# Optimization experiments

Measured on AMD Instinct MI355X. Metric: run time of the kernel, lower is better.

Reference implementation:

```python
import jax, jax.numpy as jnp
import numpy as np

EMBED = 2048
N_HEAD = 32
N_KV = 8
HEAD_DIM = 64
GROUP = N_HEAD // N_KV


def _rope_tables(seq_len, head_dim):
    inv_freq = 1.0 / (10000.0 ** (jnp.arange(0, head_dim, 2, dtype=jnp.float32) / head_dim))
    ang = jnp.arange(seq_len, dtype=jnp.float32)[:, None] * inv_freq[None, :]  # [S, D/2]
    ang = jnp.concatenate([ang, ang], axis=-1)  # [S, D]
    return jnp.cos(ang), jnp.sin(ang)


def apply_rope(x, cos, sin, offset=0):
    # x: [B, H, S, D]
    S, D = x.shape[2], x.shape[3]
    x1, x2 = x[..., : D // 2], x[..., D // 2 :]
    c = cos[offset : offset + S][None, None]
    s = sin[offset : offset + S][None, None]
    rotated = jnp.concatenate([-x2, x1], axis=-1)
    return (x * c + rotated * s).astype(x.dtype)


def setup_inputs() -> dict:
    key = jax.random.key(0)
    kx, kq, kk, kv, ko = jax.random.split(key, 5)
    B, S = 2, 2048
    x = jax.random.normal(kx, (B, S, EMBED), dtype=jnp.float32)
    mask = jnp.triu(jnp.ones((S, S), dtype=bool), k=1)  # causal: True = masked
    cos, sin = _rope_tables(S, HEAD_DIM)
    std = 0.02
    Wq = jax.random.normal(kq, (EMBED, EMBED), dtype=jnp.float32) * std
    Wk = jax.random.normal(kk, (EMBED, N_KV * HEAD_DIM), dtype=jnp.float32) * std
    Wv = jax.random.normal(kv, (EMBED, N_KV * HEAD_DIM), dtype=jnp.float32) * std
    Wo = jax.random.normal(ko, (EMBED, EMBED), dtype=jnp.float32) * std
    return {"x": x, "mask": mask, "cos": cos, "sin": sin,
            "Wq": Wq, "Wk": Wk, "Wv": Wv, "Wo": Wo}


def reference(x, mask, cos, sin, Wq, Wk, Wv, Wo):
    B, S, E = x.shape
    # projections (no bias)
    q = (x @ Wq).reshape(B, S, N_HEAD, HEAD_DIM).transpose(0, 2, 1, 3)  # [B,H,S,D]
    k = (x @ Wk).reshape(B, S, N_KV, HEAD_DIM).transpose(0, 2, 1, 3)    # [B,G,S,D]
    v = (x @ Wv).reshape(B, S, N_KV, HEAD_DIM).transpose(0, 2, 1, 3)    # [B,G,S,D]
    q = apply_rope(q, cos, sin, offset=0)
    k = apply_rope(k, cos, sin, offset=0)
    next_k, next_v = k, v  # kv cache to return
    # GQA: head h uses kv group h // GROUP; avoid repeat_interleave via reshape
    qg = q.reshape(B, N_KV, GROUP, S, HEAD_DIM)
    scores = jnp.einsum('bgjsd,bgtd->bgjst', qg, k) / np.float32(np.sqrt(HEAD_DIM))
    scores = jnp.where(mask[None, None, None], -jnp.inf, scores)
    attn = jax.nn.softmax(scores, axis=-1)
    out = jnp.einsum('bgjst,bgtd->bgjsd', attn, v)          # [B,G,group,S,D]
    out = out.reshape(B, N_HEAD, S, HEAD_DIM).transpose(0, 2, 1, 3).reshape(B, S, E)
    return out @ Wo, next_k, next_v
```

## Files before the change

### kernel.cpp

```cpp
#include <hip/hip_runtime.h>
#include <hip/hip_bf16.h>
#include <math.h>

#define NH 32
#define NKV 8
#define HD 64
#define B_ 2
#define S_ 2048
#define E_ 2048
#define M_ 4096

typedef unsigned short ushort_t;
typedef __attribute__((ext_vector_type(8))) short short8;
typedef __attribute__((ext_vector_type(4))) short short4v;
typedef __attribute__((ext_vector_type(4))) float floatx4;

__device__ inline unsigned short f2bf(float f) {
  unsigned int u = __float_as_uint(f);
  return (unsigned short)((u + 0x7FFFu + ((u >> 16) & 1u)) >> 16);
}

__device__ inline float fexp2(float x) {
  float r;
  asm("v_exp_f32 %0, %1" : "=v"(r) : "v"(x));
  return r;
}

__device__ inline void ld_lds16(const void* g, void* l) {
  __builtin_amdgcn_global_load_lds((__attribute__((address_space(1))) void*)g,
                                   (__attribute__((address_space(3))) void*)l, 16, 0, 0);
}

__device__ inline void transp32(const float* __restrict__ in, ushort_t* __restrict__ out,
                                int R, int C, int bx, int by, int tid, float (*tile)[33]) {
  int c0 = bx * 32, r0 = by * 32;
  int x = tid & 31, y0 = tid >> 5;
  for (int i = 0; i < 4; i++) {
    int r = y0 + i * 8;
    tile[r][x] = in[(size_t)(r0 + r) * C + c0 + x];
  }
  __syncthreads();
  for (int i = 0; i < 4; i++) {
    int r = y0 + i * 8;
    out[(size_t)(c0 + r) * R + r0 + x] = f2bf(tile[x][r]);
  }
}

__global__ __launch_bounds__(256) void prep(const float* __restrict__ x,
                                            ushort_t* __restrict__ xb,
                                            const float* __restrict__ Wq,
                                            const float* __restrict__ Wk,
                                            const float* __restrict__ Wv,
                                            ushort_t* __restrict__ WT) {
  __shared__ float tile[32][33];
  int bid = blockIdx.x, tid = threadIdx.x;
  if (bid < 4096) {
    size_t i = ((size_t)bid * 256 + tid) * 8;
    float4 a = *(const float4*)(x + i);
    float4 b = *(const float4*)(x + i + 4);
    short8 o;
    o[0] = (short)f2bf(a.x); o[1] = (short)f2bf(a.y);
    o[2] = (short)f2bf(a.z); o[3] = (short)f2bf(a.w);
    o[4] = (short)f2bf(b.x); o[5] = (short)f2bf(b.y);
    o[6] = (short)f2bf(b.z); o[7] = (short)f2bf(b.w);
    *(short8*)(xb + i) = o;
    return;
  }
  bid -= 4096;
  if (bid < 4096) { transp32(Wq, WT, 2048, 2048, bid & 63, bid >> 6, tid, tile); return; }
  bid -= 4096;
  if (bid < 1024) { transp32(Wk, WT + 2048 * 2048, 2048, 512, bid & 15, bid >> 4, tid, tile); return; }
  bid -= 1024;
  transp32(Wv, WT + 2560 * 2048, 2048, 512, bid & 15, bid >> 4, tid, tile);
}

__global__ __launch_bounds__(512) void gemm_qkv(const ushort_t* __restrict__ xb,
                                                const ushort_t* __restrict__ WT,
                                                ushort_t* __restrict__ qbf,
                                                float* __restrict__ outk,
                                                ushort_t* __restrict__ kbf,
                                                float* __restrict__ outv,
                                                ushort_t* __restrict__ vt,
                                                const float* __restrict__ cosP,
                                                const float* __restrict__ sinP) {
  __shared__ __align__(16) ushort_t L8[2][2][2][128][64];
  char* Lb = (char*)L8;
  int bid = blockIdx.x;
  int xcd = bid & 7, ii = bid >> 3;
  int mg = xcd >> 1, ng = xcd & 1;
  int m0 = (mg * 4 + ii / 6) * 256;
  int n0 = (ng * 6 + ii % 6) * 256;
  int tid = threadIdx.x;
  int w8 = tid >> 6, lane = tid & 63;
  int wrq = w8 >> 1, wcq = w8 & 1;
  int lr = lane & 15, quad = lane >> 4;
  int sx = lr & 7;
  int srow = w8 * 16 + (lane >> 3);
  int schunk = (lane & 7) ^ (lane >> 3);
  const char* abase = (const char*)(xb + (size_t)m0 * 2048);
  const char* bbase = (const char*)(WT + (size_t)n0 * 2048);
  floatx4 acc[4][2][4] = {};

#define STG(T, U)                                                                        \
  do {                                                                                   \
    const int mat_ = (U)&1, half_ = (U) >> 1;                                            \
    const char* sp = (mat_ ? bbase : abase) + (size_t)(half_ * 128 + srow) * 4096 +      \
                     (size_t)(T)*128 + schunk * 16;                                      \
    char* dp = Lb + (((T)&1) * 65536) + mat_ * 32768 + half_ * 16384 + w8 * 2048;        \
    ld_lds16(sp, dp);                                                                    \
    ld_lds16(sp + (size_t)8 * 4096, dp + 1024);                                          \
  } while (0)

#define PH(T, P, MH_, NH_, WAITS, DOSTAGE)                                               \
  do {                                                                                   \
    asm volatile(WAITS ::: "memory");                                                    \
    const char* Ab_ = Lb + (((T)&1) * 65536) + (MH_)*16384;                              \
    const char* Bb_ = Lb + (((T)&1) * 65536) + 32768 + (NH_)*16384;                      \
    short8 af_[2][2], bf_[4][2];                                                         \
    _Pragma("unroll") for (int i = 0; i < 2; i++) {                                      \
      size_t rb = (size_t)(wrq * 32 + i * 16 + lr) * 128;                                \
      _Pragma("unroll") for (int ks = 0; ks < 2; ks++)                                   \
          af_[i][ks] = *(const short8*)(Ab_ + rb + (((ks * 4 + quad) ^ sx) << 4));       \
    }                                                                                    \
    _Pragma("unroll") for (int j = 0; j < 4; j++) {                                      \
      size_t rb = (size_t)(wcq * 64 + j * 16 + lr) * 128;                                \
      _Pragma("unroll") for (int ks = 0; ks < 2; ks++)                                   \
          bf_[j][ks] = *(const short8*)(Bb_ + rb + (((ks * 4 + quad) ^ sx) << 4));       \
    }                                                                                    \
    if (DOSTAGE) STG((T) + 1, P);                                                        \
    __builtin_amdgcn_s_setprio(1);                                                       \
    _Pragma("unroll") for (int i = 0; i < 2; i++) _Pragma("unroll") for (int j = 0;      \
                                                                         j < 4; j++) {  \
      acc[P][i][j] =                                                                     \
          __builtin_amdgcn_mfma_f32_16x16x32_bf16(af_[i][0], bf_[j][0], acc[P][i][j],    \
                                                  0, 0, 0);                              \
      acc[P][i][j] =                                                                     \
          __builtin_amdgcn_mfma_f32_16x16x32_bf16(af_[i][1], bf_[j][1], acc[P][i][j],    \
                                                  0, 0, 0);                              \
    }                                                                                    \
    __builtin_amdgcn_s_setprio(0);                                                       \
  } while (0)

  STG(0, 0); STG(0, 1); STG(0, 2); STG(0, 3);

  for (int kt = 0; kt < 31; kt++) {
    PH(kt, 0, 0, 0, "s_waitcnt vmcnt(4)\n\ts_barrier", 1);
    PH(kt, 1, 1, 0, "s_waitcnt vmcnt(4)\n\ts_barrier", 1);
    PH(kt, 2, 1, 1, "s_waitcnt vmcnt(4)\n\ts_barrier", 1);
    PH(kt, 3, 0, 1, "s_barrier", 1);
  }
  PH(31, 0, 0, 0, "s_waitcnt vmcnt(4)\n\ts_barrier", 0);
  PH(31, 1, 1, 0, "s_waitcnt vmcnt(2)\n\ts_barrier", 0);
  PH(31, 2, 1, 1, "s_waitcnt vmcnt(0)\n\ts_barrier", 0);
  PH(31, 3, 0, 1, "s_barrier", 0);
#undef STG
#undef PH

  const int MHs[4] = {0, 1, 1, 0}, NHs[4] = {0, 0, 1, 1};
  if (n0 < 2048) {
    const float QS = 0.125f * 1.4426950408889634f;
#pragma unroll
    for (int p = 0; p < 4; p++)
#pragma unroll
      for (int i = 0; i < 2; i++)
#pragma unroll
        for (int j = 0; j < 2; j++) {
          int d = j * 16 + lr;
#pragma unroll
          for (int r = 0; r < 4; r++) {
            int row = m0 + MHs[p] * 128 + wrq * 32 + i * 16 + quad * 4 + r;
            int s = row & (S_ - 1);
            float c = cosP[s * 64 + d], sn = sinP[s * 64 + d];
            float x1 = acc[p][i][j][r], x2 = acc[p][i][j + 2][r];
            size_t oo = (size_t)row * 2048 + n0 + NHs[p] * 128 + wcq * 64 + d;
            qbf[oo] = f2bf((x1 * c - x2 * sn) * QS);
            qbf[oo + 32] = f2bf((x2 * c + x1 * sn) * QS);
          }
        }
  } else if (n0 < 2560) {
#pragma unroll
    for (int p = 0; p < 4; p++) {
      int h = ((n0 - 2048) >> 6) + NHs[p] * 2 + wcq;
#pragma unroll
      for (int i = 0; i < 2; i++)
#pragma unroll
        for (int j = 0; j < 2; j++) {
          int d = j * 16 + lr;
#pragma unroll
          for (int r = 0; r < 4; r++) {
            int row = m0 + MHs[p] * 128 + wrq * 32 + i * 16 + quad * 4 + r;
            int s = row & (S_ - 1), b = row >> 11;
            float c = cosP[s * 64 + d], sn = sinP[s * 64 + d];
            float x1 = acc[p][i][j][r], x2 = acc[p][i][j + 2][r];
            float y1 = x1 * c - x2 * sn, y2 = x2 * c + x1 * sn;
            size_t rowb = ((size_t)(b * NKV + h) * S_ + s) * 64;
            int xr = (s & 7) << 3;
            outk[rowb + d] = y1; outk[rowb + d + 32] = y2;
            kbf[rowb + (d ^ xr)] = f2bf(y1);
            kbf[rowb + ((d + 32) ^ xr)] = f2bf(y2);
          }
        }
    }
  } else {
#pragma unroll
    for (int p = 0; p < 4; p++) {
      int h = ((n0 - 2560) >> 6) + NHs[p] * 2 + wcq;
#pragma unroll
      for (int i = 0; i < 2; i++)
#pragma unroll
        for (int j = 0; j < 4; j++) {
          int d = j * 16 + lr;
          int row0 = m0 + MHs[p] * 128 + wrq * 32 + i * 16 + quad * 4;
          int s0 = row0 & (S_ - 1), b = row0 >> 11;
#pragma unroll
          for (int r = 0; r < 4; r++)
            outv[((size_t)(b * NKV + h) * S_ + s0 + r) * 64 + d] = acc[p][i][j][r];
          int tt = s0 >> 6, s4 = s0 & 63;
          short4v u;
          u[0] = (short)f2bf(acc[p][i][j][0]); u[1] = (short)f2bf(acc[p][i][j][1]);
          u[2] = (short)f2bf(acc[p][i][j][2]); u[3] = (short)f2bf(acc[p][i][j][3]);
          *(short4v*)(vt + ((size_t)(b * NKV + h) * 32 + tt) * 4096 + d * 64 +
                      (s4 ^ ((d & 7) << 3))) = u;
        }
    }
  }
}

__device__ __forceinline__ void gemm128_core(const ushort_t* __restrict__ Ag,
                                             const ushort_t* __restrict__ Bg,
                                             floatx4 (&acc)[4][4]) {
  __shared__ __align__(16) ushort_t As[2][128][64];
  __shared__ __align__(16) ushort_t Bs[2][128][64];
  int tid = threadIdx.x;
  int w = tid >> 6, lane = tid & 63;
  int wm = (w >> 1) * 64, wn = (w & 1) * 64;
  int lr = lane & 15, quad = lane >> 4;
  int sx = lr & 7;
  char* Asb = (char*)As;
  char* Bsb = (char*)Bs;

  size_t so[4];
#pragma unroll
  for (int s = 0; s < 4; s++)
    so[s] = (size_t)(w * 32 + s * 8 + (lane >> 3)) * 4096 + (size_t)(((lane & 7) ^ (lane >> 3)) * 16);
  const char* abase = (const char*)Ag;
  const char* bbase = (const char*)Bg;

#define STAGE128(buf, kt)                                          \
  do {                                                             \
    size_t ko = (size_t)(kt) * 128;                                \
    char* Ad = Asb + (buf) * 16384 + w * 4096;                     \
    char* Bd = Bsb + (buf) * 16384 + w * 4096;                     \
    _Pragma("unroll") for (int s = 0; s < 4; s++) {                \
      ld_lds16(abase + so[s] + ko, Ad + s * 1024);                 \
      ld_lds16(bbase + so[s] + ko, Bd + s * 1024);                 \
    }                                                              \
  } while (0)

  STAGE128(0, 0);
  __syncthreads();

  int cur = 0;
  for (int kt = 0; kt < 32; kt++) {
    if (kt < 31) STAGE128(cur ^ 1, kt + 1);
    const char* Ab = Asb + cur * 16384;
    const char* Bb = Bsb + cur * 16384;
    short8 af[4][2], bfr[4][2];
#pragma unroll
    for (int i = 0; i < 4; i++) {
      size_t rb = (size_t)(wm + i * 16 + lr) * 128;
#pragma unroll
      for (int ks = 0; ks < 2; ks++)
        af[i][ks] = *(const short8*)(Ab + rb + (((ks * 4 + quad) ^ sx) << 4));
    }
#pragma unroll
    for (int j = 0; j < 4; j++) {
      size_t rb = (size_t)(wn + j * 16 + lr) * 128;
#pragma unroll
      for (int ks = 0; ks < 2; ks++)
        bfr[j][ks] = *(const short8*)(Bb + rb + (((ks * 4 + quad) ^ sx) << 4));
    }
#pragma unroll
    for (int i = 0; i < 4; i++)
#pragma unroll
      for (int j = 0; j < 4; j++) {
        acc[i][j] = __builtin_amdgcn_mfma_f32_16x16x32_bf16(af[i][0], bfr[j][0], acc[i][j], 0, 0, 0);
        acc[i][j] = __builtin_amdgcn_mfma_f32_16x16x32_bf16(af[i][1], bfr[j][1], acc[i][j], 0, 0, 0);
      }
    __syncthreads();
    cur ^= 1;
  }
#undef STAGE128
}

__global__ __launch_bounds__(256) void gemm_o(const ushort_t* __restrict__ ctx,
                                              const ushort_t* __restrict__ WoT,
                                              float* __restrict__ y) {
  int o = blockIdx.y * 16 + blockIdx.x;
  int xcd = o & 7, i = o >> 3;
  int mg = xcd >> 1, ng = xcd & 1;
  int m0 = (mg * 8 + (i >> 3)) * 128;
  int n0 = (ng * 8 + (i & 7)) * 128;
  int tid = threadIdx.x;
  int w = tid >> 6, lane = tid & 63;
  int wm = (w >> 1) * 64, wn = (w & 1) * 64;
  int lr = lane & 15, quad = lane >> 4;

  floatx4 acc[4][4] = {};
  gemm128_core(ctx + (size_t)m0 * 2048, WoT + (size_t)n0 * 2048, acc);

#pragma unroll
  for (int i2 = 0; i2 < 4; i2++)
#pragma unroll
    for (int j = 0; j < 4; j++) {
      int row = m0 + wm + i2 * 16 + quad * 4;
      int col = n0 + wn + j * 16 + lr;
#pragma unroll
      for (int r = 0; r < 4; r++)
        y[(size_t)(row + r) * 2048 + col] = acc[i2][j][r];
    }
}

__global__ __launch_bounds__(256, 3) void attn2(ushort_t* __restrict__ q,
                                                const ushort_t* __restrict__ k,
                                                const ushort_t* __restrict__ vt,
                                                const float* __restrict__ Wo,
                                                ushort_t* __restrict__ WoT) {
  __shared__ __align__(16) ushort_t KV[2][2][64][64];
  __shared__ __align__(16) ushort_t Ps[4][2][16][64];
  __shared__ float tile[32][33];
  int bid0 = blockIdx.x;
  int tid = threadIdx.x;
  if (bid0 >= 1024) {
    int bid2 = bid0 - 1024;
    transp32(Wo, WoT, 2048, 2048, bid2 & 63, bid2 >> 6, tid, tile);
    return;
  }
  int bh = bid0 & 63;
  int qi = 15 - (bid0 >> 6);
  int b = bh >> 5, h = bh & 31, g = h >> 2;
  int w = tid >> 6, lane = tid & 63;
  int lr = lane & 15, quad = lane >> 4;

  int qg0 = qi * 128 + w * 16 + lr;
  int qg1 = qg0 + 64;
  short8 a00, a01, a10, a11;
  {
    const ushort_t* qp0 = q + ((size_t)(b * S_ + qg0) * NH + h) * HD;
    const ushort_t* qp1 = q + ((size_t)(b * S_ + qg1) * NH + h) * HD;
    a00 = *(const short8*)(qp0 + quad * 8);
    a01 = *(const short8*)(qp0 + 32 + quad * 8);
    a10 = *(const short8*)(qp1 + quad * 8);
    a11 = *(const short8*)(qp1 + 32 + quad * 8);
  }
  floatx4 od0[4] = {}, od1[4] = {};
  float mi0 = -INFINITY, li0 = 0.f, mi1 = -INFINITY, li1 = 0.f;

  const char* ksrc = (const char*)(k + (size_t)(b * NKV + g) * S_ * HD) + w * 2048 + lane * 16;
  const char* vsrc = (const char*)(vt + (size_t)(b * NKV + g) * S_ * HD) + w * 2048 + lane * 16;
  char* dB = (char*)&KV[0][0][0][0] + w * 2048;

  int sw = (lr & 7) << 4;
  int ro0 = (quad * 16) ^ sw;
  int ro1 = (64 + quad * 16) ^ sw;
  char* Pw = (char*)&Ps[0][0][0][0] + w * 4096;

  ld_lds16(ksrc, dB);
  ld_lds16(ksrc + 1024, dB + 1024);
  ld_lds16(vsrc, dB + 8192);
  ld_lds16(vsrc + 1024, dB + 8192 + 1024);
  asm volatile("s_waitcnt vmcnt(0)" ::: "memory");
  __syncthreads();

  int T = 2 * qi + 2;
  int cur = 0;
  for (int t = 0; t < T; t++) {
    if (t + 1 < T) {
      const char* kn = ksrc + (size_t)(t + 1) * 8192;
      const char* vn = vsrc + (size_t)(t + 1) * 8192;
      char* d = dB + (cur ^ 1) * 16384;
      ld_lds16(kn, d); ld_lds16(kn + 1024, d + 1024);
      ld_lds16(vn, d + 8192); ld_lds16(vn + 1024, d + 8192 + 1024);
    }
    const char* Kb = (const char*)&KV[cur][0][0][0];
    const char* Vb = (const char*)&KV[cur][1][0][0];
    bool dq0 = (t == 2 * qi);
    bool skip0 = (t == 2 * qi + 1);
    if (!skip0) {
      floatx4 sc[4];
      __builtin_amdgcn_s_setprio(1);
#pragma unroll
      for (int kn = 0; kn < 4; kn++) {
        short8 k0 = *(const short8*)(Kb + (kn * 16 + lr) * 128 + ro0);
        short8 k1 = *(const short8*)(Kb + (kn * 16 + lr) * 128 + ro1);
        floatx4 c = {};
        c = __builtin_amdgcn_mfma_f32_16x16x32_bf16(k0, a00, c, 0, 0, 0);
        c = __builtin_amdgcn_mfma_f32_16x16x32_bf16(k1, a01, c, 0, 0, 0);
        sc[kn] = c;
      }
      __builtin_amdgcn_s_setprio(0);
      float pv[16];
#pragma unroll
      for (int kn = 0; kn < 4; kn++)
#pragma unroll
        for (int r = 0; r < 4; r++) pv[kn * 4 + r] = sc[kn][r];
      if (dq0) {
#pragma unroll
        for (int e = 0; e < 16; e++) {
          int kg = t * 64 + (e >> 2) * 16 + quad * 4 + (e & 3);
          if (kg > qg0) pv[e] = -INFINITY;
        }
      }
      float m01 = fmaxf(pv[0], pv[1]),  m23 = fmaxf(pv[2], pv[3]);
      float m45 = fmaxf(pv[4], pv[5]),  m67 = fmaxf(pv[6], pv[7]);
      float m89 = fmaxf(pv[8], pv[9]),  mab = fmaxf(pv[10], pv[11]);
      float mcd = fmaxf(pv[12], pv[13]), mef = fmaxf(pv[14], pv[15]);
      float mx = fmaxf(fmaxf(fmaxf(m01, m23), fmaxf(m45, m67)),
                       fmaxf(fmaxf(m89, mab), fmaxf(mcd, mef)));
      mx = fmaxf(mx, __shfl_xor(mx, 16));
      mx = fmaxf(mx, __shfl_xor(mx, 32));
      if (__any(mx > mi0 + 11.5f)) {
        float mn = fmaxf(mi0, mx);
        float al = fexp2(mi0 - mn);
        li0 *= al;
#pragma unroll
        for (int dn = 0; dn < 4; dn++) {
          od0[dn][0] *= al; od0[dn][1] *= al; od0[dn][2] *= al; od0[dn][3] *= al;
        }
        mi0 = mn;
      }
      float ps = 0.f;
#pragma unroll
      for (int e = 0; e < 16; e++) {
        pv[e] = fexp2(pv[e] - mi0);
        ps += pv[e];
      }
      ps += __shfl_xor(ps, 16);
      ps += __shfl_xor(ps, 32);
      li0 += ps;
#pragma unroll
      for (int kn = 0; kn < 4; kn++) {
        unsigned int u0, u1;
        asm("v_cvt_pk_bf16_f32 %0, %1, %2" : "=v"(u0) : "v"(pv[kn * 4 + 0]), "v"(pv[kn * 4 + 1]));
        asm("v_cvt_pk_bf16_f32 %0, %1, %2" : "=v"(u1) : "v"(pv[kn * 4 + 2]), "v"(pv[kn * 4 + 3]));
        uint2 uu; uu.x = u0; uu.y = u1;
        *(uint2*)(Pw + lr * 128 + ((kn * 32 + quad * 8) ^ sw)) = uu;
      }
    }
    {
      floatx4 sc[4];
      __builtin_amdgcn_s_setprio(1);
#pragma unroll
      for (int kn = 0; kn < 4; kn++) {
        short8 k0 = *(const short8*)(Kb + (kn * 16 + lr) * 128 + ro0);
        short8 k1 = *(const short8*)(Kb + (kn * 16 + lr) * 128 + ro1);
        floatx4 c = {};
        c = __builtin_amdgcn_mfma_f32_16x16x32_bf16(k0, a10, c, 0, 0, 0);
        c = __builtin_amdgcn_mfma_f32_16x16x32_bf16(k1, a11, c, 0, 0, 0);
        sc[kn] = c;
      }
      __builtin_amdgcn_s_setprio(0);
      float pv[16];
#pragma unroll
      for (int kn = 0; kn < 4; kn++)
#pragma unroll
        for (int r = 0; r < 4; r++) pv[kn * 4 + r] = sc[kn][r];
      if (skip0) {
#pragma unroll
        for (int e = 0; e < 16; e++) {
          int kg = t * 64 + (e >> 2) * 16 + quad * 4 + (e & 3);
          if (kg > qg1) pv[e] = -INFINITY;
        }
      }
      float m01 = fmaxf(pv[0], pv[1]),  m23 = fmaxf(pv[2], pv[3]);
      float m45 = fmaxf(pv[4], pv[5]),  m67 = fmaxf(pv[6], pv[7]);
      float m89 = fmaxf(pv[8], pv[9]),  mab = fmaxf(pv[10], pv[11]);
      float mcd = fmaxf(pv[12], pv[13]), mef = fmaxf(pv[14], pv[15]);
      float mx = fmaxf(fmaxf(fmaxf(m01, m23), fmaxf(m45, m67)),
                       fmaxf(fmaxf(m89, mab), fmaxf(mcd, mef)));
      mx = fmaxf(mx, __shfl_xor(mx, 16));
      mx = fmaxf(mx, __shfl_xor(mx, 32));
      if (__any(mx > mi1 + 11.5f)) {
        float mn = fmaxf(mi1, mx);
        float al = fexp2(mi1 - mn);
        li1 *= al;
#pragma unroll
        for (int dn = 0; dn < 4; dn++) {
          od1[dn][0] *= al; od1[dn][1] *= al; od1[dn][2] *= al; od1[dn][3] *= al;
        }
        mi1 = mn;
      }
      float ps = 0.f;
#pragma unroll
      for (int e = 0; e < 16; e++) {
        pv[e] = fexp2(pv[e] - mi1);
        ps += pv[e];
      }
      ps += __shfl_xor(ps, 16);
      ps += __shfl_xor(ps, 32);
      li1 += ps;
#pragma unroll
      for (int kn = 0; kn < 4; kn++) {
        unsigned int u0, u1;
        asm("v_cvt_pk_bf16_f32 %0, %1, %2" : "=v"(u0) : "v"(pv[kn * 4 + 0]), "v"(pv[kn * 4 + 1]));
        asm("v_cvt_pk_bf16_f32 %0, %1, %2" : "=v"(u1) : "v"(pv[kn * 4 + 2]), "v"(pv[kn * 4 + 3]));
        uint2 uu; uu.x = u0; uu.y = u1;
        *(uint2*)(Pw + 2048 + lr * 128 + ((kn * 32 + quad * 8) ^ sw)) = uu;
      }
    }
    __builtin_amdgcn_s_setprio(1);
    if (!skip0) {
      short8 pb0 = *(const short8*)(Pw + lr * 128 + ro0);
      short8 pb1 = *(const short8*)(Pw + lr * 128 + ro1);
#pragma unroll
      for (int dn = 0; dn < 4; dn++) {
        short8 va = *(const short8*)(Vb + (dn * 16 + lr) * 128 + ro0);
        short8 vb = *(const short8*)(Vb + (dn * 16 + lr) * 128 + ro1);
        od0[dn] = __builtin_amdgcn_mfma_f32_16x16x32_bf16(va, pb0, od0[dn], 0, 0, 0);
        od0[dn] = __builtin_amdgcn_mfma_f32_16x16x32_bf16(vb, pb1, od0[dn], 0, 0, 0);
      }
    }
    {
      short8 pb0 = *(const short8*)(Pw + 2048 + lr * 128 + ro0);
      short8 pb1 = *(const short8*)(Pw + 2048 + lr * 128 + ro1);
#pragma unroll
      for (int dn = 0; dn < 4; dn++) {
        short8 va = *(const short8*)(Vb + (dn * 16 + lr) * 128 + ro0);
        short8 vb = *(const short8*)(Vb + (dn * 16 + lr) * 128 + ro1);
        od1[dn] = __builtin_amdgcn_mfma_f32_16x16x32_bf16(va, pb0, od1[dn], 0, 0, 0);
        od1[dn] = __builtin_amdgcn_mfma_f32_16x16x32_bf16(vb, pb1, od1[dn], 0, 0, 0);
      }
    }
    __builtin_amdgcn_s_setprio(0);
    asm volatile("s_waitcnt vmcnt(0)" ::: "memory");
    __syncthreads();
    cur ^= 1;
  }
  float inv0 = 1.f / li0, inv1 = 1.f / li1;
  ushort_t* outp0 = q + ((size_t)(b * S_ + qg0) * NH + h) * HD;
  ushort_t* outp1 = q + ((size_t)(b * S_ + qg1) * NH + h) * HD;
#pragma unroll
  for (int dn = 0; dn < 4; dn++) {
    short4v u;
    u[0] = (short)f2bf(od0[dn][0] * inv0); u[1] = (short)f2bf(od0[dn][1] * inv0);
    u[2] = (short)f2bf(od0[dn][2] * inv0); u[3] = (short)f2bf(od0[dn][3] * inv0);
    *(short4v*)(outp0 + dn * 16 + quad * 4) = u;
    short4v v;
    v[0] = (short)f2bf(od1[dn][0] * inv1); v[1] = (short)f2bf(od1[dn][1] * inv1);
    v[2] = (short)f2bf(od1[dn][2] * inv1); v[3] = (short)f2bf(od1[dn][3] * inv1);
    *(short4v*)(outp1 + dn * 16 + quad * 4) = v;
  }
}

extern "C" void kernel_launch(void* const* d_in, const int* in_sizes, int n_in,
                              void* d_out, int out_size, void* d_ws, size_t ws_size,
                              hipStream_t stream) {
  const float* x = (const float*)d_in[0];
  const float* cosT = (const float*)d_in[2];
  const float* sinT = (const float*)d_in[3];
  const float* Wq = (const float*)d_in[4];
  const float* Wk = (const float*)d_in[5];
  const float* Wv = (const float*)d_in[6];
  const float* Wo = (const float*)d_in[7];

  char* ws = (char*)d_ws;
  ushort_t* WT = (ushort_t*)(ws);
  ushort_t* WoT = (ushort_t*)(ws + 12582912);
  ushort_t* xb = (ushort_t*)(ws + 20971520);
  ushort_t* qbf = (ushort_t*)(ws + 37748736);
  ushort_t* kbf = (ushort_t*)(ws + 54525952);
  ushort_t* vt = (ushort_t*)(ws + 58720256);

  float* y = (float*)d_out;
  float* outk = y + (size_t)M_ * E_;
  float* outv = outk + (size_t)B_ * NKV * S_ * HD;

  prep<<<dim3(10240), 256, 0, stream>>>(x, xb, Wq, Wk, Wv, WT);

  gemm_qkv<<<dim3(192), 512, 0, stream>>>(xb, WT, qbf, outk, kbf, outv, vt, cosT, sinT);

  attn2<<<dim3(5120), 256, 0, stream>>>(qbf, kbf, vt, Wo, WoT);

  gemm_o<<<dim3(16, 32), 256, 0, stream>>>(qbf, WoT, y);
}
```

Measured before the change: 305.8 us.

## Use partial vmcnt waits for KV prefetch and share K/V fragment loads across rows

Moves the wait for the next KV tile to the top of each iteration using vmcnt(4) plus a raw s_barrier, so the prefetch for tile t+1 stays in flight while tile t is computed. The trailing full vmcnt(0) wait is dropped. The QK^T and PV MFMA loops for the two query row blocks are merged so each K and V fragment is read from LDS once and used for both. This reduces LDS reads and exposed global-load latency, but raises register pressure and depends on the exact count of outstanding loads being correct.

```diff
diff --git a/kernel.cpp b/kernel.cpp
--- a/kernel.cpp
+++ b/kernel.cpp
@@ -365,45 +365,54 @@
   int ro1 = (64 + quad * 16) ^ sw;
   char* Pw = (char*)&Ps[0][0][0][0] + w * 4096;
 
-  ld_lds16(ksrc, dB);
-  ld_lds16(ksrc + 1024, dB + 1024);
-  ld_lds16(vsrc, dB + 8192);
-  ld_lds16(vsrc + 1024, dB + 8192 + 1024);
-  asm volatile("s_waitcnt vmcnt(0)" ::: "memory");
-  __syncthreads();
+#define ASTG(t, d)                                                   \
+  do {                                                               \
+    const char* kn_ = ksrc + (size_t)(t) * 8192;                     \
+    const char* vn_ = vsrc + (size_t)(t) * 8192;                     \
+    ld_lds16(kn_, d); ld_lds16(kn_ + 1024, (char*)(d) + 1024);       \
+    ld_lds16(vn_, (char*)(d) + 8192);                                \
+    ld_lds16(vn_ + 1024, (char*)(d) + 8192 + 1024);                  \
+  } while (0)
+
+  ASTG(0, dB);
 
   int T = 2 * qi + 2;
   int cur = 0;
   for (int t = 0; t < T; t++) {
     if (t + 1 < T) {
-      const char* kn = ksrc + (size_t)(t + 1) * 8192;
-      const char* vn = vsrc + (size_t)(t + 1) * 8192;
-      char* d = dB + (cur ^ 1) * 16384;
-      ld_lds16(kn, d); ld_lds16(kn + 1024, d + 1024);
-      ld_lds16(vn, d + 8192); ld_lds16(vn + 1024, d + 8192 + 1024);
+      ASTG(t + 1, dB + (cur ^ 1) * 16384);
+      asm volatile("s_waitcnt vmcnt(4)\n\ts_barrier" ::: "memory");
+    } else {
+      asm volatile("s_waitcnt vmcnt(0)\n\ts_barrier" ::: "memory");
     }
     const char* Kb = (const char*)&KV[cur][0][0][0];
     const char* Vb = (const char*)&KV[cur][1][0][0];
     bool dq0 = (t == 2 * qi);
     bool skip0 = (t == 2 * qi + 1);
+    floatx4 sc0[4], sc1[4];
+    __builtin_amdgcn_s_setprio(1);
+#pragma unroll
+    for (int kn = 0; kn < 4; kn++) {
+      short8 k0 = *(const short8*)(Kb + (kn * 16 + lr) * 128 + ro0);
+      short8 k1 = *(const short8*)(Kb + (kn * 16 + lr) * 128 + ro1);
+      floatx4 c1 = {};
+      c1 = __builtin_amdgcn_mfma_f32_16x16x32_bf16(k0, a10, c1, 0, 0, 0);
+      c1 = __builtin_amdgcn_mfma_f32_16x16x32_bf16(k1, a11, c1, 0, 0, 0);
+      sc1[kn] = c1;
+      if (!skip0) {
+        floatx4 c0 = {};
+        c0 = __builtin_amdgcn_mfma_f32_16x16x32_bf16(k0, a00, c0, 0, 0, 0);
+        c0 = __builtin_amdgcn_mfma_f32_16x16x32_bf16(k1, a01, c0, 0, 0, 0);
+        sc0[kn] = c0;
+      }
+    }
+    __builtin_amdgcn_s_setprio(0);
     if (!skip0) {
-      floatx4 sc[4];
-      __builtin_amdgcn_s_setprio(1);
-#pragma unroll
-      for (int kn = 0; kn < 4; kn++) {
-        short8 k0 = *(const short8*)(Kb + (kn * 16 + lr) * 128 + ro0);
-        short8 k1 = *(const short8*)(Kb + (kn * 16 + lr) * 128 + ro1);
-        floatx4 c = {};
-        c = __builtin_amdgcn_mfma_f32_16x16x32_bf16(k0, a00, c, 0, 0, 0);
-        c = __builtin_amdgcn_mfma_f32_16x16x32_bf16(k1, a01, c, 0, 0, 0);
-        sc[kn] = c;
-      }
-      __builtin_amdgcn_s_setprio(0);
       float pv[16];
 #pragma unroll
       for (int kn = 0; kn < 4; kn++)
 #pragma unroll
-        for (int r = 0; r < 4; r++) pv[kn * 4 + r] = sc[kn][r];
+        for (int r = 0; r < 4; r++) pv[kn * 4 + r] = sc0[kn][r];
       if (dq0) {
 #pragma unroll
         for (int e = 0; e < 16; e++) {
@@ -448,23 +457,11 @@
       }
     }
     {
-      floatx4 sc[4];
-      __builtin_amdgcn_s_setprio(1);
-#pragma unroll
-      for (int kn = 0; kn < 4; kn++) {
-        short8 k0 = *(const short8*)(Kb + (kn * 16 + lr) * 128 + ro0);
-        short8 k1 = *(const short8*)(Kb + (kn * 16 + lr) * 128 + ro1);
-        floatx4 c = {};
-        c = __builtin_amdgcn_mfma_f32_16x16x32_bf16(k0, a10, c, 0, 0, 0);
-        c = __builtin_amdgcn_mfma_f32_16x16x32_bf16(k1, a11, c, 0, 0, 0);
-        sc[kn] = c;
-      }
-      __builtin_amdgcn_s_setprio(0);
       float pv[16];
 #pragma unroll
       for (int kn = 0; kn < 4; kn++)
 #pragma unroll
-        for (int r = 0; r < 4; r++) pv[kn * 4 + r] = sc[kn][r];
+        for (int r = 0; r < 4; r++) pv[kn * 4 + r] = sc1[kn][r];
       if (skip0) {
 #pragma unroll
         for (int e = 0; e < 16; e++) {
@@ -508,34 +505,30 @@
         *(uint2*)(Pw + 2048 + lr * 128 + ((kn * 32 + quad * 8) ^ sw)) = uu;
       }
     }
+    short8 pb00, pb01, pb10, pb11;
+    if (!skip0) {
+      pb00 = *(const short8*)(Pw + lr * 128 + ro0);
+      pb01 = *(const short8*)(Pw + lr * 128 + ro1);
+    }
+    pb10 = *(const short8*)(Pw + 2048 + lr * 128 + ro0);
+    pb11 = *(const short8*)(Pw + 2048 + lr * 128 + ro1);
     __builtin_amdgcn_s_setprio(1);
-    if (!skip0) {
-      short8 pb0 = *(const short8*)(Pw + lr * 128 + ro0);
-      short8 pb1 = *(const short8*)(Pw + lr * 128 + ro1);
-#pragma unroll
-      for (int dn = 0; dn < 4; dn++) {
-        short8 va = *(const short8*)(Vb + (dn * 16 + lr) * 128 + ro0);
-        short8 vb = *(const short8*)(Vb + (dn * 16 + lr) * 128 + ro1);
-        od0[dn] = __builtin_amdgcn_mfma_f32_16x16x32_bf16(va, pb0, od0[dn], 0, 0, 0);
-        od0[dn] = __builtin_amdgcn_mfma_f32_16x16x32_bf16(vb, pb1, od0[dn], 0, 0, 0);
-      }
-    }
-    {
-      short8 pb0 = *(const short8*)(Pw + 2048 + lr * 128 + ro0);
-      short8 pb1 = *(const short8*)(Pw + 2048 + lr * 128 + ro1);
-#pragma unroll
-      for (int dn = 0; dn < 4; dn++) {
-        short8 va = *(const short8*)(Vb + (dn * 16 + lr) * 128 + ro0);
-        short8 vb = *(const short8*)(Vb + (dn * 16 + lr) * 128 + ro1);
-        od1[dn] = __builtin_amdgcn_mfma_f32_16x16x32_bf16(va, pb0, od1[dn], 0, 0, 0);
-        od1[dn] = __builtin_amdgcn_mfma_f32_16x16x32_bf16(vb, pb1, od1[dn], 0, 0, 0);
+#pragma unroll
+    for (int dn = 0; dn < 4; dn++) {
+      short8 va = *(const short8*)(Vb + (dn * 16 + lr) * 128 + ro0);
+      short8 vb = *(const short8*)(Vb + (dn * 16 + lr) * 128 + ro1);
+      od1[dn] = __builtin_amdgcn_mfma_f32_16x16x32_bf16(va, pb10, od1[dn], 0, 0, 0);
+      od1[dn] = __builtin_amdgcn_mfma_f32_16x16x32_bf16(vb, pb11, od1[dn], 0, 0, 0);
+      if (!skip0) {
+        od0[dn] = __builtin_amdgcn_mfma_f32_16x16x32_bf16(va, pb00, od0[dn], 0, 0, 0);
+        od0[dn] = __builtin_amdgcn_mfma_f32_16x16x32_bf16(vb, pb01, od0[dn], 0, 0, 0);
       }
     }
     __builtin_amdgcn_s_setprio(0);
-    asm volatile("s_waitcnt vmcnt(0)" ::: "memory");
-    __syncthreads();
+    asm volatile("s_barrier" ::: "memory");
     cur ^= 1;
   }
+#undef ASTG
   float inv0 = 1.f / li0, inv1 = 1.f / li1;
   ushort_t* outp0 = q + ((size_t)(b * S_ + qg0) * NH + h) * HD;
   ushort_t* outp1 = q + ((size_t)(b * S_ + qg1) * NH + h) * HD;
```

New measurement: 307.2 us. Within noise of the previous version (+0.5%).
